# Kernel optimization log

Measured on AMD Instinct MI355X. Metric: run time of the kernel, lower is better.

The kernel has to match this reference:

```python
import jax, jax.numpy as jnp
import numpy as np

B_, J_, D_, E_, N_, K_ = 32, 1024, 192, 384, 16, 3


def _dwconv(x, w, b):
    # x: (B,J,E), w: (E,1,K) depthwise, b: (E,)
    xc = jnp.transpose(x, (0, 2, 1))  # (B,E,J)
    pad = w.shape[2] // 2
    y = jax.lax.conv_general_dilated(
        xc, w, window_strides=(1,), padding=[(pad, pad)],
        feature_group_count=w.shape[0], dimension_numbers=('NCH', 'OIH', 'NCH'))
    return jnp.transpose(y + b[None, :, None], (0, 2, 1))  # (B,J,E)


def _scan_dir(x, cw, cb, WB, bB, WC, bC, WD, bD, A, Wi, bi, Wr, br):
    # One directional selective-SSM pass. x: (B,J,E); A: (N,) negative diag.
    xc = _dwconv(x, cw, cb)                       # (B,J,E)
    Bt = xc @ WB + bB                             # (B,J,N)
    Ct = xc @ WC + bC                             # (B,J,N)
    Dt = jax.nn.softplus(xc @ WD + bD)            # Delta, (B,J,N)
    A_bar = jnp.exp(Dt * A)                       # ZOH discretization
    B_bar = (A_bar - 1.0) / (A + 1e-6) * Bt
    u = xc @ Wi + bi                              # in_to_state, (B,J,N)
    Bu = B_bar * u

    def step(h, ab_bu):
        ab, bu = ab_bu
        h = ab * h + bu
        return h, h

    h0 = jnp.zeros((x.shape[0], A.shape[0]), x.dtype)
    _, hs = jax.lax.scan(step, h0, (jnp.swapaxes(A_bar, 0, 1), jnp.swapaxes(Bu, 0, 1)))
    hs = jnp.swapaxes(hs, 0, 1)                   # (B,J,N)
    return (hs * Ct) @ Wr + br                    # readout, (B,J,E)


def setup_inputs() -> dict:
    key = jax.random.key(0)
    ks = iter(jax.random.split(key, 40))

    def nrm(shape, scale=0.02):
        return jax.random.normal(next(ks), shape, jnp.float32) * scale

    inp = {
        'tokens': jax.random.normal(next(ks), (B_, J_, D_), jnp.float32),
        'norm_g': jnp.ones((D_,), jnp.float32),
        'norm_b': jnp.zeros((D_,), jnp.float32),
        'Wx': nrm((D_, E_)), 'bx': jnp.zeros((E_,), jnp.float32),
        'Wz': nrm((D_, E_)), 'bz': jnp.zeros((E_,), jnp.float32),
        'convf_w': nrm((E_, 1, K_), 0.1), 'convf_b': jnp.zeros((E_,), jnp.float32),
        'convb_w': nrm((E_, 1, K_), 0.1), 'convb_b': jnp.zeros((E_,), jnp.float32),
        'WBf': nrm((E_, N_)), 'bBf': jnp.zeros((N_,), jnp.float32),
        'WCf': nrm((E_, N_)), 'bCf': jnp.zeros((N_,), jnp.float32),
        'WDf': nrm((E_, N_)), 'bDf': jnp.zeros((N_,), jnp.float32),
        'WBb': nrm((E_, N_)), 'bBb': jnp.zeros((N_,), jnp.float32),
        'WCb': nrm((E_, N_)), 'bCb': jnp.zeros((N_,), jnp.float32),
        'WDb': nrm((E_, N_)), 'bDb': jnp.zeros((N_,), jnp.float32),
        'A_log': nrm((N_,), 0.5),
        'Wi': nrm((E_, N_)), 'bi': jnp.zeros((N_,), jnp.float32),
        'Wr': nrm((N_, E_)), 'br': jnp.zeros((E_,), jnp.float32),
        'Wo': nrm((E_, D_)), 'bo': jnp.zeros((D_,), jnp.float32),
    }
    return inp


def reference(tokens, norm_g, norm_b, Wx, bx, Wz, bz, convf_w, convf_b,
              convb_w, convb_b, WBf, bBf, WCf, bCf, WDf, bDf, WBb, bBb,
              WCb, bCb, WDb, bDb, A_log, Wi, bi, Wr, br, Wo, bo):
    # LayerNorm (biased variance, eps=1e-5, like torch)
    mu = jnp.mean(tokens, axis=-1, keepdims=True)
    var = jnp.mean(jnp.square(tokens - mu), axis=-1, keepdims=True)
    t = (tokens - mu) / jnp.sqrt(var + 1e-5) * norm_g + norm_b

    x = t @ Wx + bx
    z = t @ Wz + bz
    gate = jax.nn.sigmoid(jax.nn.silu(z))

    # A computed under no_grad in torch -> stop_gradient here
    A = jax.lax.stop_gradient(-jax.nn.softplus(A_log))

    y_f = _scan_dir(x, convf_w, convf_b, WBf, bBf, WCf, bCf, WDf, bDf, A, Wi, bi, Wr, br)
    y_b = jnp.flip(_scan_dir(jnp.flip(x, 1), convb_w, convb_b, WBb, bBb, WCb, bCb,
                             WDb, bDb, A, Wi, bi, Wr, br), 1)
    y = (y_f + y_b) * gate
    return tokens + y @ Wo + bo
```

## Files before the change

kernel.cpp:

```cpp
#include <hip/hip_runtime.h>
#include <math.h>


typedef __attribute__((ext_vector_type(8))) short short8;
typedef __attribute__((ext_vector_type(4))) float f32x4;

__device__ __forceinline__ unsigned short f2bf(float f){
  union { float f; unsigned u; } v; v.f = f;
  unsigned r = v.u + 0x7FFFu + ((v.u >> 16) & 1u);
  return (unsigned short)(r >> 16);
}
__device__ __forceinline__ float bf2f(unsigned short s){
  union { unsigned u; float f; } v; v.u = ((unsigned)s) << 16;
  return v.f;
}
__device__ __forceinline__ float softplusf(float x){
  return (x > 20.f) ? x : log1pf(expf(x));
}
__device__ __forceinline__ float sigf_fast(float x){
  return __builtin_amdgcn_rcpf(1.f + __expf(-x));
}

__global__ __launch_bounds__(256) void prep_kernel(
    const float* __restrict__ Wx, const float* __restrict__ Wz,
    const float* __restrict__ WBf, const float* __restrict__ WCf,
    const float* __restrict__ WDf, const float* __restrict__ WBb,
    const float* __restrict__ WCb, const float* __restrict__ WDb,
    const float* __restrict__ Wi, const float* __restrict__ Wr,
    const float* __restrict__ Wo,
    const float* __restrict__ bBf, const float* __restrict__ bCf,
    const float* __restrict__ bDf, const float* __restrict__ bBb,
    const float* __restrict__ bCb, const float* __restrict__ bDb,
    const float* __restrict__ bi,
    unsigned short* __restrict__ Wxz_t, unsigned short* __restrict__ W4f_t,
    unsigned short* __restrict__ W4b_t, unsigned short* __restrict__ Wrt2,
    unsigned short* __restrict__ Wot, float* __restrict__ b4f,
    float* __restrict__ b4b)
{
  int idx = blockIdx.x * 256 + threadIdx.x;
  if (idx < 147456){ int n = idx / 192, k = idx % 192;
    Wxz_t[idx] = f2bf(n < 384 ? Wx[k*384 + n] : Wz[k*384 + n - 384]); return; }
  idx -= 147456;
  if (idx < 24576){ int n = idx / 384, k = idx % 384;
    const float* W = (n<16)?WBf:(n<32)?WCf:(n<48)?WDf:Wi;
    W4f_t[idx] = f2bf(W[k*16 + (n&15)]); return; }
  idx -= 24576;
  if (idx < 24576){ int n = idx / 384, k = idx % 384;
    const float* W = (n<16)?WBb:(n<32)?WCb:(n<48)?WDb:Wi;
    W4b_t[idx] = f2bf(W[k*16 + (n&15)]); return; }
  idx -= 24576;
  if (idx < 12288){ int n = idx / 32, k = idx % 32;
    Wrt2[idx] = f2bf(Wr[(k&15)*384 + n]); return; }
  idx -= 12288;
  if (idx < 73728){ int n = idx / 384, k = idx % 384;
    Wot[idx] = f2bf(Wo[k*192 + n]); return; }
  idx -= 73728;
  if (idx < 64){
    const float* bsel = (idx<16)?bBf:(idx<32)?bCf:(idx<48)?bDf:bi;
    b4f[idx] = bsel[idx & 15]; return; }
  idx -= 64;
  if (idx < 64){
    const float* bsel = (idx<16)?bBb:(idx<32)?bCb:(idx<48)?bDb:bi;
    b4b[idx] = bsel[idx & 15]; return; }
}

__global__ __launch_bounds__(512) void ln_xz_mfma(
    const float* __restrict__ tokens, const float* __restrict__ g,
    const float* __restrict__ nb, const unsigned short* __restrict__ Wxz_t,
    const float* __restrict__ bx, const float* __restrict__ bz,
    unsigned short* __restrict__ x_bf, unsigned short* __restrict__ gate_bf)
{
  __shared__ unsigned short t_lds[32 * 200];
  __shared__ unsigned short out_lds[32 * 784];
  const int t = threadIdx.x;
  const int row0 = blockIdx.x * 32;

  {
    const int r = t >> 4, l16 = t & 15;
    const float* tr = tokens + (long)(row0 + r) * 192;
    float v[12], s = 0.f, sq = 0.f;
#pragma unroll
    for (int i = 0; i < 12; i++){ float x = tr[l16 + 16*i]; v[i] = x; s += x; sq += x*x; }
#pragma unroll
    for (int m = 1; m < 16; m <<= 1){ s += __shfl_xor(s, m); sq += __shfl_xor(sq, m); }
    const float mu = s * (1.f/192.f);
    const float rstd = rsqrtf(sq * (1.f/192.f) - mu*mu + 1e-5f);
#pragma unroll
    for (int i = 0; i < 12; i++){
      const int d = l16 + 16*i;
      t_lds[r*200 + d] = f2bf((v[i] - mu)*rstd*g[d] + nb[d]);
    }
  }
  __syncthreads();

  const int lane = t & 63, w = t >> 6;
  const int c0 = w * 96;
  const int l15 = lane & 15, q = lane >> 4;
  f32x4 acc[2][6];
#pragma unroll
  for (int m = 0; m < 2; m++)
#pragma unroll
    for (int n = 0; n < 6; n++) acc[m][n] = (f32x4){0.f,0.f,0.f,0.f};

  const unsigned short* wb = Wxz_t + (long)(c0 + l15)*192 + q*8;
#pragma unroll
  for (int ks = 0; ks < 6; ks++){
    const int k0 = ks * 32;
    short8 a0 = *(const short8*)&t_lds[l15*200 + k0 + q*8];
    short8 a1 = *(const short8*)&t_lds[(16 + l15)*200 + k0 + q*8];
#pragma unroll
    for (int nf = 0; nf < 6; nf++){
      short8 bw = *(const short8*)&wb[nf*16*192 + k0];
      acc[0][nf] = __builtin_amdgcn_mfma_f32_16x16x32_bf16(a0, bw, acc[0][nf], 0, 0, 0);
      acc[1][nf] = __builtin_amdgcn_mfma_f32_16x16x32_bf16(a1, bw, acc[1][nf], 0, 0, 0);
    }
  }

#pragma unroll
  for (int nf = 0; nf < 6; nf++){
    const int c = c0 + nf*16 + l15;
    const int scol = c0 + ((nf + q) % 6)*16 + l15;
    if (c < 384){
      const float bv = bx[c];
#pragma unroll
      for (int m = 0; m < 2; m++)
#pragma unroll
        for (int r = 0; r < 4; r++){
          const int row = m*16 + q*4 + r;
          out_lds[row*784 + scol] = f2bf(acc[m][nf][r] + bv);
        }
    } else {
      const float bv = bz[c - 384];
#pragma unroll
      for (int m = 0; m < 2; m++)
#pragma unroll
        for (int r = 0; r < 4; r++){
          const int row = m*16 + q*4 + r;
          const float z = acc[m][nf][r] + bv;
          const float si = z * sigf_fast(z);
          out_lds[row*784 + scol] = f2bf(sigf_fast(si));
        }
    }
  }
  __syncthreads();

  {
#pragma unroll
    for (int i = 0; i < 6; i++){
      const int item = i*512 + t;
      const int row  = item / 96;
      const int cblk = item % 96;
      const int c_out = cblk * 8;
      const int qq = (row >> 2) & 3;
      const int ws = c_out / 96;
      const int nfl = (c_out % 96) / 16;
      const int scol = ws*96 + ((nfl + qq) % 6)*16 + (c_out % 16);
      short8 v = *(const short8*)&out_lds[row*784 + scol];
      const long R = (long)row0 + row;
      if (c_out < 384) *(short8*)&x_bf[R*384 + c_out] = v;
      else             *(short8*)&gate_bf[R*384 + (c_out - 384)] = v;
    }
  }
}

__global__ __launch_bounds__(256) void proj_mfma(
    const unsigned short* __restrict__ x_bf,
    const float* __restrict__ cwf, const float* __restrict__ cbf,
    const float* __restrict__ cwb, const float* __restrict__ cbb,
    const unsigned short* __restrict__ W4f, const unsigned short* __restrict__ W4b,
    const float* __restrict__ b4f, const float* __restrict__ b4b,
    const float* __restrict__ A_log,
    float* __restrict__ Af, float* __restrict__ Buf, float* __restrict__ Ctf,
    float* __restrict__ Ab, float* __restrict__ Bub, float* __restrict__ Ctb)
{
  __shared__ unsigned short xc[64 * 392];
  float* trans = (float*)xc;
  const int t = threadIdx.x;
  const int dir = blockIdx.x >> 9;
  const int bid = blockIdx.x & 511;
  const int b  = bid >> 4;
  const int j0 = (bid & 15) * 64;
  const float* cw = dir ? cwb : cwf;
  const float* cb = dir ? cbb : cbf;
  const unsigned short* W4 = dir ? W4b : W4f;
  const float* b4 = dir ? b4b : b4f;
  float* Aout = dir ? Ab  : Af;
  float* Bout = dir ? Bub : Buf;
  float* Cout = dir ? Ctb : Ctf;

  {
    const long xrow = (long)b * 1024 * 384;
#pragma unroll
    for (int i = 0; i < 12; i++){
      const int idx = i*256 + t;
      const int r = idx / 48;
      const int e0 = (idx - r*48) * 8;
      const int jp = j0 + r;
      short8 xm = (short8){0,0,0,0,0,0,0,0};
      short8 xp = (short8){0,0,0,0,0,0,0,0};
      if (jp >= 1){
        const int js = dir ? 1024 - jp : jp - 1;
        xm = *(const short8*)&x_bf[xrow + (long)js*384 + e0];
      }
      short8 x0;
      {
        const int js = dir ? 1023 - jp : jp;
        x0 = *(const short8*)&x_bf[xrow + (long)js*384 + e0];
      }
      if (jp <= 1022){
        const int js = dir ? 1022 - jp : jp + 1;
        xp = *(const short8*)&x_bf[xrow + (long)js*384 + e0];
      }
      float wv[24], cbv[8];
#pragma unroll
      for (int v = 0; v < 6; v++)
        *(float4*)&wv[v*4] = *(const float4*)&cw[e0*3 + v*4];
#pragma unroll
      for (int v = 0; v < 2; v++)
        *(float4*)&cbv[v*4] = *(const float4*)&cb[e0 + v*4];
      short8 o;
#pragma unroll
      for (int m = 0; m < 8; m++){
        const float acc = fmaf(wv[3*m],   bf2f((unsigned short)xm[m]),
                          fmaf(wv[3*m+1], bf2f((unsigned short)x0[m]),
                          fmaf(wv[3*m+2], bf2f((unsigned short)xp[m]), cbv[m])));
        o[m] = (short)f2bf(acc);
      }
      *(short8*)&xc[r*392 + e0] = o;
    }
  }
  __syncthreads();

  const int lane = t & 63, w = t >> 6;
  const int l15 = lane & 15, q = lane >> 4;
  f32x4 acc[4];
#pragma unroll
  for (int nf = 0; nf < 4; nf++) acc[nf] = (f32x4){0.f,0.f,0.f,0.f};
  const unsigned short* wb = W4 + (long)l15*384 + q*8;
#pragma unroll
  for (int ks = 0; ks < 12; ks++){
    const int k0 = ks * 32;
    short8 a = *(const short8*)&xc[(w*16 + l15)*392 + k0 + q*8];
#pragma unroll
    for (int nf = 0; nf < 4; nf++){
      short8 bw = *(const short8*)&wb[nf*16*384 + k0];
      acc[nf] = __builtin_amdgcn_mfma_f32_16x16x32_bf16(a, bw, acc[nf], 0, 0, 0);
    }
  }
  __syncthreads();

  {
    const int n = l15;
    const float Av = -softplusf(A_log[n]);
    const float bB = b4[n], bC = b4[16+n], bD = b4[32+n], bU = b4[48+n];
#pragma unroll
    for (int r = 0; r < 4; r++){
      const int row = w*16 + q*4 + r;
      const float Bt  = acc[0][r] + bB;
      const float Ctv = acc[1][r] + bC;
      const float dt  = softplusf(acc[2][r] + bD);
      const float u   = acc[3][r] + bU;
      const float ab  = expf(dt * Av);
      const float bu  = (ab - 1.f) / (Av + 1e-6f) * Bt * u;
      trans[(0*16 + n)*66 + row] = ab;
      trans[(1*16 + n)*66 + row] = bu;
      trans[(2*16 + n)*66 + row] = Ctv;
    }
  }
  __syncthreads();

  {
    const int j = t & 63, n4 = t >> 6;
#pragma unroll
    for (int i = 0; i < 4; i++){
      const int n = n4*4 + i;
      const int jp = j0 + j;
      const long base = ((long)b*16 + n) * 1024;
      Aout[base + jp] = trans[(0*16 + n)*66 + j];
      Bout[base + jp] = trans[(1*16 + n)*66 + j];
      Cout[base + (dir ? 1023 - jp : jp)] = trans[(2*16 + n)*66 + j];
    }
  }
}

__global__ __launch_bounds__(256) void scan2_kernel(
    const float* __restrict__ Af, const float* __restrict__ Buf, float* __restrict__ hsf,
    const float* __restrict__ Ab, const float* __restrict__ Bub, float* __restrict__ hsb)
{
  __shared__ float sA[256], sB[256];
  const int sel = blockIdx.x >> 9;
  const long base = (long)(blockIdx.x & 511) * 1024;
  const float* Abar = sel ? Ab  : Af;
  const float* Bu   = sel ? Bub : Buf;
  float* hs         = sel ? hsb : hsf;
  const int t = threadIdx.x;
  const float4 a4 = *reinterpret_cast<const float4*>(&Abar[base + t*4]);
  const float4 b4 = *reinterpret_cast<const float4*>(&Bu[base + t*4]);
  float A = a4.x, Bc = b4.x;
  Bc = fmaf(a4.y, Bc, b4.y); A *= a4.y;
  Bc = fmaf(a4.z, Bc, b4.z); A *= a4.z;
  Bc = fmaf(a4.w, Bc, b4.w); A *= a4.w;
  sA[t] = A; sB[t] = Bc;
  __syncthreads();
  for (int off = 1; off < 256; off <<= 1){
    const float cA = sA[t], cB = sB[t];
    float pA = 1.f, pB = 0.f;
    if (t >= off){ pA = sA[t - off]; pB = sB[t - off]; }
    __syncthreads();
    sA[t] = pA * cA;
    sB[t] = fmaf(cA, pB, cB);
    __syncthreads();
  }
  float h = (t > 0) ? sB[t - 1] : 0.f;
  float4 o;
  h = fmaf(a4.x, h, b4.x); o.x = h;
  h = fmaf(a4.y, h, b4.y); o.y = h;
  h = fmaf(a4.z, h, b4.z); o.z = h;
  h = fmaf(a4.w, h, b4.w); o.w = h;
  *reinterpret_cast<float4*>(&hs[base + t*4]) = o;
}

__global__ __launch_bounds__(256) void final_mfma(
    const float* __restrict__ tokens, const unsigned short* __restrict__ gate_bf,
    const float* __restrict__ hsf, const float* __restrict__ Ctf,
    const float* __restrict__ hsb, const float* __restrict__ Ctb,
    const unsigned short* __restrict__ Wrt2, const float* __restrict__ br,
    const unsigned short* __restrict__ Wot, const float* __restrict__ bo,
    float* __restrict__ out)
{
  __shared__ unsigned short s2[64 * 40];
  __shared__ unsigned short yg[64 * 392];
  const int t = threadIdx.x;
  const int b  = blockIdx.x >> 4;
  const int j0 = (blockIdx.x & 15) * 64;

  {
    const int j = t & 63, grp = t >> 6;
#pragma unroll
    for (int i = 0; i < 8; i++){
      const int kk = grp*8 + i;
      float val;
      if (kk < 16){
        const long p = ((long)b*16 + kk)*1024 + j0 + j;
        val = hsf[p] * Ctf[p];
      } else {
        const long basen = ((long)b*16 + (kk - 16)) * 1024;
        val = hsb[basen + 1023 - (j0 + j)] * Ctb[basen + j0 + j];
      }
      s2[j*40 + kk] = f2bf(val);
    }
  }
  __syncthreads();

  const int lane = t & 63, w = t >> 6;
  const int l15 = lane & 15, q = lane >> 4;

  {
    short8 a = *(const short8*)&s2[(w*16 + l15)*40 + q*8];
    const unsigned short* wbp = Wrt2 + (long)l15*32 + q*8;
#pragma unroll
    for (int nf = 0; nf < 24; nf++){
      short8 bw = *(const short8*)&wbp[nf*16*32];
      f32x4 acc = (f32x4){0.f,0.f,0.f,0.f};
      acc = __builtin_amdgcn_mfma_f32_16x16x32_bf16(a, bw, acc, 0, 0, 0);
      const int c = nf*16 + l15;
      const float brv = 2.f * br[c];
#pragma unroll
      for (int r = 0; r < 4; r++){
        const int row = w*16 + q*4 + r;
        yg[row*392 + c] = f2bf(acc[r] + brv);
      }
    }
  }
  __syncthreads();

  {
#pragma unroll
    for (int i = 0; i < 12; i++){
      const int item = i*256 + t;
      const int row = item / 48;
      const int cb  = (item % 48) * 8;
      short8 y8 = *(const short8*)&yg[row*392 + cb];
      short8 g8 = *(const short8*)&gate_bf[((long)b*1024 + j0 + row)*384 + cb];
      short8 o;
#pragma unroll
      for (int m = 0; m < 8; m++)
        o[m] = (short)f2bf(bf2f((unsigned short)y8[m]) * bf2f((unsigned short)g8[m]));
      *(short8*)&yg[row*392 + cb] = o;
    }
  }
  __syncthreads();

  f32x4 acc[12];
  {
#pragma unroll
    for (int nf = 0; nf < 12; nf++) acc[nf] = (f32x4){0.f,0.f,0.f,0.f};
    const unsigned short* wbp = Wot + (long)l15*384 + q*8;
#pragma unroll
    for (int ks = 0; ks < 12; ks++){
      const int k0 = ks * 32;
      short8 a = *(const short8*)&yg[(w*16 + l15)*392 + k0 + q*8];
#pragma unroll
      for (int nf = 0; nf < 12; nf++){
        short8 bw = *(const short8*)&wbp[(long)nf*16*384 + k0];
        acc[nf] = __builtin_amdgcn_mfma_f32_16x16x32_bf16(a, bw, acc[nf], 0, 0, 0);
      }
    }
  }
  __syncthreads();

  float* stg = (float*)yg;
  {
    const int gq = q ^ (q >> 1);
#pragma unroll
    for (int nf = 0; nf < 12; nf++){
      const int c = nf*16 + l15;
      const float bv = bo[c];
      const int scol = ((nf + gq) % 12)*16 + l15;
#pragma unroll
      for (int r = 0; r < 4; r++){
        const int row = w*16 + q*4 + r;
        stg[row*196 + scol] = acc[nf][r] + bv;
      }
    }
  }
  __syncthreads();

  {
#pragma unroll
    for (int i = 0; i < 12; i++){
      const int item = i*256 + t;
      const int row = item / 48;
      const int c4  = (item % 48) * 4;
      const int qq = (row >> 2) & 3;
      const int gg = qq ^ (qq >> 1);
      const int nf = c4 / 16;
      const int scol = ((nf + gg) % 12)*16 + (c4 % 16);
      float4 v = *(const float4*)&stg[row*196 + scol];
      const long R = (long)b*1024 + j0 + row;
      const float4 tk = *(const float4*)&tokens[R*192 + c4];
      v.x += tk.x; v.y += tk.y; v.z += tk.z; v.w += tk.w;
      *(float4*)&out[R*192 + c4] = v;
    }
  }
}

extern "C" void kernel_launch(void* const* d_in, const int* in_sizes, int n_in,
                              void* d_out, int out_size, void* d_ws, size_t ws_size,
                              hipStream_t stream)
{
  const float* tokens  = (const float*)d_in[0];
  const float* norm_g  = (const float*)d_in[1];
  const float* norm_b  = (const float*)d_in[2];
  const float* Wx      = (const float*)d_in[3];
  const float* bx      = (const float*)d_in[4];
  const float* Wz      = (const float*)d_in[5];
  const float* bz      = (const float*)d_in[6];
  const float* convf_w = (const float*)d_in[7];
  const float* convf_b = (const float*)d_in[8];
  const float* convb_w = (const float*)d_in[9];
  const float* convb_b = (const float*)d_in[10];
  const float* WBf     = (const float*)d_in[11];
  const float* bBf     = (const float*)d_in[12];
  const float* WCf     = (const float*)d_in[13];
  const float* bCf     = (const float*)d_in[14];
  const float* WDf     = (const float*)d_in[15];
  const float* bDf     = (const float*)d_in[16];
  const float* WBb     = (const float*)d_in[17];
  const float* bBb     = (const float*)d_in[18];
  const float* WCb     = (const float*)d_in[19];
  const float* bCb     = (const float*)d_in[20];
  const float* WDb     = (const float*)d_in[21];
  const float* bDb     = (const float*)d_in[22];
  const float* A_log   = (const float*)d_in[23];
  const float* Wi      = (const float*)d_in[24];
  const float* bi      = (const float*)d_in[25];
  const float* Wr      = (const float*)d_in[26];
  const float* br      = (const float*)d_in[27];
  const float* Wo      = (const float*)d_in[28];
  const float* bo      = (const float*)d_in[29];

  char* ws = (char*)d_ws;
  unsigned short* x_bf    = (unsigned short*)(ws + 0);
  unsigned short* gate_bf = (unsigned short*)(ws + 25165824);
  unsigned short* Wxz_t   = (unsigned short*)(ws + 50331648);
  unsigned short* W4f_t   = (unsigned short*)(ws + 50626560);
  unsigned short* W4b_t   = (unsigned short*)(ws + 50675712);
  unsigned short* Wrt2    = (unsigned short*)(ws + 50724864);
  unsigned short* Wot     = (unsigned short*)(ws + 50749440);
  float* b4f = (float*)(ws + 50896896);
  float* b4b = (float*)(ws + 50897152);
  float* Af  = (float*)(ws + 50897408);
  float* Buf = (float*)(ws + 52994560);
  float* Ctf = (float*)(ws + 55091712);
  float* hsf = (float*)(ws + 57188864);
  float* Ab  = (float*)(ws + 59286016);
  float* Bub = (float*)(ws + 61383168);
  float* Ctb = (float*)(ws + 63480320);
  float* hsb = (float*)(ws + 65577472);

  prep_kernel<<<1105, 256, 0, stream>>>(Wx, Wz, WBf, WCf, WDf, WBb, WCb, WDb,
                                        Wi, Wr, Wo, bBf, bCf, bDf, bBb, bCb, bDb, bi,
                                        Wxz_t, W4f_t, W4b_t, Wrt2, Wot, b4f, b4b);
  ln_xz_mfma<<<1024, 512, 0, stream>>>(tokens, norm_g, norm_b, Wxz_t, bx, bz,
                                       x_bf, gate_bf);
  proj_mfma<<<1024, 256, 0, stream>>>(x_bf, convf_w, convf_b, convb_w, convb_b,
                                      W4f_t, W4b_t, b4f, b4b, A_log,
                                      Af, Buf, Ctf, Ab, Bub, Ctb);
  scan2_kernel<<<1024, 256, 0, stream>>>(Af, Buf, hsf, Ab, Bub, hsb);
  final_mfma<<<512, 256, 0, stream>>>(tokens, gate_bf, hsf, Ctf, hsb, Ctb,
                                      Wrt2, br, Wot, bo, (float*)d_out);
}
```

Measured before the change: 152.3 us.

## Halve LDS staging in ln_xz and shrink final_mfma tiles to 32 rows

```diff
diff --git a/kernel.cpp b/kernel.cpp
--- a/kernel.cpp
+++ b/kernel.cpp
@@ -71,7 +71,7 @@
     unsigned short* __restrict__ x_bf, unsigned short* __restrict__ gate_bf)
 {
   __shared__ unsigned short t_lds[32 * 200];
-  __shared__ unsigned short out_lds[32 * 784];
+  __shared__ unsigned short out_lds[16 * 784];
   const int t = threadIdx.x;
   const int row0 = blockIdx.x * 32;
 
@@ -117,49 +117,44 @@
   }
 
 #pragma unroll
-  for (int nf = 0; nf < 6; nf++){
-    const int c = c0 + nf*16 + l15;
-    const int scol = c0 + ((nf + q) % 6)*16 + l15;
-    if (c < 384){
-      const float bv = bx[c];
-#pragma unroll
-      for (int m = 0; m < 2; m++)
+  for (int m = 0; m < 2; m++){
+#pragma unroll
+    for (int nf = 0; nf < 6; nf++){
+      const int c = c0 + nf*16 + l15;
+      const int scol = c0 + ((nf + q) % 6)*16 + l15;
+      if (c < 384){
+        const float bv = bx[c];
+#pragma unroll
+        for (int r = 0; r < 4; r++)
+          out_lds[(q*4 + r)*784 + scol] = f2bf(acc[m][nf][r] + bv);
+      } else {
+        const float bv = bz[c - 384];
 #pragma unroll
         for (int r = 0; r < 4; r++){
-          const int row = m*16 + q*4 + r;
-          out_lds[row*784 + scol] = f2bf(acc[m][nf][r] + bv);
-        }
-    } else {
-      const float bv = bz[c - 384];
-#pragma unroll
-      for (int m = 0; m < 2; m++)
-#pragma unroll
-        for (int r = 0; r < 4; r++){
-          const int row = m*16 + q*4 + r;
           const float z = acc[m][nf][r] + bv;
           const float si = z * sigf_fast(z);
-          out_lds[row*784 + scol] = f2bf(sigf_fast(si));
+          out_lds[(q*4 + r)*784 + scol] = f2bf(sigf_fast(si));
         }
-    }
-  }
-  __syncthreads();
-
-  {
-#pragma unroll
-    for (int i = 0; i < 6; i++){
-      const int item = i*512 + t;
-      const int row  = item / 96;
-      const int cblk = item % 96;
-      const int c_out = cblk * 8;
-      const int qq = (row >> 2) & 3;
-      const int ws = c_out / 96;
-      const int nfl = (c_out % 96) / 16;
-      const int scol = ws*96 + ((nfl + qq) % 6)*16 + (c_out % 16);
-      short8 v = *(const short8*)&out_lds[row*784 + scol];
-      const long R = (long)row0 + row;
-      if (c_out < 384) *(short8*)&x_bf[R*384 + c_out] = v;
-      else             *(short8*)&gate_bf[R*384 + (c_out - 384)] = v;
-    }
+      }
+    }
+    __syncthreads();
+    {
+#pragma unroll
+      for (int i = 0; i < 3; i++){
+        const int item = i*512 + t;
+        const int row  = item / 96;
+        const int c_out = (item % 96) * 8;
+        const int qq = (row >> 2) & 3;
+        const int wsl = c_out / 96;
+        const int nfl = (c_out % 96) / 16;
+        const int scol = wsl*96 + ((nfl + qq) % 6)*16 + (c_out % 16);
+        short8 v = *(const short8*)&out_lds[row*784 + scol];
+        const long R = (long)row0 + m*16 + row;
+        if (c_out < 384) *(short8*)&x_bf[R*384 + c_out] = v;
+        else             *(short8*)&gate_bf[R*384 + (c_out - 384)] = v;
+      }
+    }
+    __syncthreads();
   }
 }
 
@@ -328,17 +323,17 @@
     const unsigned short* __restrict__ Wot, const float* __restrict__ bo,
     float* __restrict__ out)
 {
-  __shared__ unsigned short s2[64 * 40];
-  __shared__ unsigned short yg[64 * 392];
+  __shared__ unsigned short s2[32 * 40];
+  __shared__ unsigned short yg[32 * 392];
   const int t = threadIdx.x;
-  const int b  = blockIdx.x >> 4;
-  const int j0 = (blockIdx.x & 15) * 64;
-
-  {
-    const int j = t & 63, grp = t >> 6;
-#pragma unroll
-    for (int i = 0; i < 8; i++){
-      const int kk = grp*8 + i;
+  const int b  = blockIdx.x >> 5;
+  const int j0 = (blockIdx.x & 31) * 32;
+
+  {
+#pragma unroll
+    for (int i = 0; i < 4; i++){
+      const int idx = i*256 + t;
+      const int j = idx & 31, kk = idx >> 5;
       float val;
       if (kk < 16){
         const long p = ((long)b*16 + kk)*1024 + j0 + j;
@@ -354,29 +349,30 @@
 
   const int lane = t & 63, w = t >> 6;
   const int l15 = lane & 15, q = lane >> 4;
-
-  {
-    short8 a = *(const short8*)&s2[(w*16 + l15)*40 + q*8];
+  const int rt = w & 1;
+  const int ng = w >> 1;
+
+  {
+    short8 a = *(const short8*)&s2[(rt*16 + l15)*40 + q*8];
     const unsigned short* wbp = Wrt2 + (long)l15*32 + q*8;
 #pragma unroll
-    for (int nf = 0; nf < 24; nf++){
+    for (int i = 0; i < 12; i++){
+      const int nf = ng*12 + i;
       short8 bw = *(const short8*)&wbp[nf*16*32];
       f32x4 acc = (f32x4){0.f,0.f,0.f,0.f};
       acc = __builtin_amdgcn_mfma_f32_16x16x32_bf16(a, bw, acc, 0, 0, 0);
       const int c = nf*16 + l15;
       const float brv = 2.f * br[c];
 #pragma unroll
-      for (int r = 0; r < 4; r++){
-        const int row = w*16 + q*4 + r;
-        yg[row*392 + c] = f2bf(acc[r] + brv);
-      }
-    }
-  }
-  __syncthreads();
-
-  {
-#pragma unroll
-    for (int i = 0; i < 12; i++){
+      for (int r = 0; r < 4; r++)
+        yg[(rt*16 + q*4 + r)*392 + c] = f2bf(acc[r] + brv);
+    }
+  }
+  __syncthreads();
+
+  {
+#pragma unroll
+    for (int i = 0; i < 6; i++){
       const int item = i*256 + t;
       const int row = item / 48;
       const int cb  = (item % 48) * 8;
@@ -391,19 +387,20 @@
   }
   __syncthreads();
 
-  f32x4 acc[12];
-  {
-#pragma unroll
-    for (int nf = 0; nf < 12; nf++) acc[nf] = (f32x4){0.f,0.f,0.f,0.f};
+  f32x4 acc[6];
+  {
+#pragma unroll
+    for (int i = 0; i < 6; i++) acc[i] = (f32x4){0.f,0.f,0.f,0.f};
     const unsigned short* wbp = Wot + (long)l15*384 + q*8;
 #pragma unroll
     for (int ks = 0; ks < 12; ks++){
       const int k0 = ks * 32;
-      short8 a = *(const short8*)&yg[(w*16 + l15)*392 + k0 + q*8];
-#pragma unroll
-      for (int nf = 0; nf < 12; nf++){
+      short8 a = *(const short8*)&yg[(rt*16 + l15)*392 + k0 + q*8];
+#pragma unroll
+      for (int i = 0; i < 6; i++){
+        const int nf = ng*6 + i;
         short8 bw = *(const short8*)&wbp[(long)nf*16*384 + k0];
-        acc[nf] = __builtin_amdgcn_mfma_f32_16x16x32_bf16(a, bw, acc[nf], 0, 0, 0);
+        acc[i] = __builtin_amdgcn_mfma_f32_16x16x32_bf16(a, bw, acc[i], 0, 0, 0);
       }
     }
   }
@@ -413,22 +410,21 @@
   {
     const int gq = q ^ (q >> 1);
 #pragma unroll
-    for (int nf = 0; nf < 12; nf++){
+    for (int i = 0; i < 6; i++){
+      const int nf = ng*6 + i;
       const int c = nf*16 + l15;
       const float bv = bo[c];
       const int scol = ((nf + gq) % 12)*16 + l15;
 #pragma unroll
-      for (int r = 0; r < 4; r++){
-        const int row = w*16 + q*4 + r;
-        stg[row*196 + scol] = acc[nf][r] + bv;
-      }
-    }
-  }
-  __syncthreads();
-
-  {
-#pragma unroll
-    for (int i = 0; i < 12; i++){
+      for (int r = 0; r < 4; r++)
+        stg[(rt*16 + q*4 + r)*196 + scol] = acc[i][r] + bv;
+    }
+  }
+  __syncthreads();
+
+  {
+#pragma unroll
+    for (int i = 0; i < 6; i++){
       const int item = i*256 + t;
       const int row = item / 48;
       const int c4  = (item % 48) * 4;
@@ -508,6 +504,6 @@
                                       W4f_t, W4b_t, b4f, b4b, A_log,
                                       Af, Buf, Ctf, Ab, Bub, Ctb);
   scan2_kernel<<<1024, 256, 0, stream>>>(Af, Buf, hsf, Ab, Bub, hsb);
-  final_mfma<<<512, 256, 0, stream>>>(tokens, gate_bf, hsf, Ctf, hsb, Ctb,
-                                      Wrt2, br, Wot, bo, (float*)d_out);
-}
+  final_mfma<<<1024, 256, 0, stream>>>(tokens, gate_bf, hsf, Ctf, hsb, Ctb,
+                                       Wrt2, br, Wot, bo, (float*)d_out);
+}
```

Measured after the change: 150.0 us. About the same (-1.5%).
